# Kernel tuning notes

Hardware: AMD Instinct MI355X
Metric: run time of the kernel (lower is better)

The kernel has to match this reference:

```python
import jax, jax.numpy as jnp
import numpy as np

N_NODES = 100000

def prelu(x, alpha):
    return jnp.where(x >= 0, x, alpha * x)

def setup_inputs() -> dict:
    key = jax.random.key(0)
    ks = jax.random.split(key, 8)
    N, E, D = N_NODES, 1600000, 128
    AX = jax.random.normal(ks[0], (N, D), dtype=jnp.float32)
    A_row = jax.random.randint(ks[1], (E,), 0, N, dtype=jnp.int32)
    A_col = jax.random.randint(ks[2], (E,), 0, N, dtype=jnp.int32)
    A_val = jax.random.uniform(ks[3], (E,), dtype=jnp.float32)
    # Xavier-uniform linear weights, zero bias (as in module init)
    lim = float(np.sqrt(6.0 / (D + D)))
    Wr_w = jax.random.uniform(ks[4], (D, D), minval=-lim, maxval=lim, dtype=jnp.float32)
    W_w = jax.random.uniform(ks[5], (D, D), minval=-lim, maxval=lim, dtype=jnp.float32)
    Wr_b = jnp.zeros((D,), dtype=jnp.float32)
    W_b = jnp.zeros((D,), dtype=jnp.float32)
    g_alpha = jnp.full((1,), 0.25, dtype=jnp.float32)    # PReLU default init
    act_alpha = jnp.full((1,), 0.25, dtype=jnp.float32)
    return {"AX": AX, "A_row": A_row, "A_col": A_col, "A_val": A_val,
            "Wr_w": Wr_w, "Wr_b": Wr_b, "W_w": W_w, "W_b": W_b,
            "g_alpha": g_alpha, "act_alpha": act_alpha}

def reference(AX, A_row, A_col, A_val, Wr_w, Wr_b, W_w, W_b, g_alpha, act_alpha):
    # h = g(Wr @ AX)  : [N, H]
    h = prelu(AX @ Wr_w.T + Wr_b, g_alpha)
    # SpMM: temp[i] = sum_{(i,j) in E} A_val * h[j]
    msgs = A_val[:, None] * h[A_col]                       # [E, H] gather
    temp = jax.ops.segment_sum(msgs, A_row, num_segments=N_NODES)
    # act(W @ temp), unsqueeze batch dim
    out = prelu(temp @ W_w.T + W_b, act_alpha)
    return out[None, :, :]
```

## Files before the change

kernel.cpp:

```cpp
#include <hip/hip_runtime.h>
#include <stdint.h>


typedef _Float16 half8 __attribute__((ext_vector_type(8)));
typedef _Float16 half4 __attribute__((ext_vector_type(4)));
typedef _Float16 half2v __attribute__((ext_vector_type(2)));
typedef float floatx4 __attribute__((ext_vector_type(4)));

#define LDK 136
#define SHIFT 5
#define NBMAX 3200
#define NBLK 256
#define SCT 1024
#define CAP 1024

__global__ __launch_bounds__(SCT)
void bucket_hist(const int* __restrict__ rows, int* __restrict__ hist_g,
                 int E, int chunk, int NB,
                 const float* __restrict__ W, _Float16* __restrict__ W16)
{
    __shared__ int lh[NBMAX];
    int tid = threadIdx.x, blk = blockIdx.x;
    if (blk == 0) {
#pragma unroll
        for (int j = 0; j < 16; ++j) W16[tid + j * 1024] = (_Float16)W[tid + j * 1024];
    }
    for (int i = tid; i < NB; i += SCT) lh[i] = 0;
    __syncthreads();
    int s = blk * chunk, e = min(E, s + chunk);
    for (int i = s + tid; i < e; i += SCT)
        atomicAdd(&lh[rows[i] >> SHIFT], 1);
    __syncthreads();
    for (int b = tid; b < NB; b += SCT)
        hist_g[b * NBLK + blk] = lh[b];
}

__global__ __launch_bounds__(256)
void scan1_fast(int* __restrict__ hist_g, int* __restrict__ tot, int NB)
{
    const int wave = threadIdx.x >> 6;
    const int lane = threadIdx.x & 63;
    const int b = blockIdx.x * 4 + wave;
    if (b >= NB) return;

    int* p = hist_g + b * NBLK + lane * 4;
    int v0 = p[0], v1 = p[1], v2 = p[2], v3 = p[3];
    int s = v0 + v1 + v2 + v3;

    int x = s;
#pragma unroll
    for (int off = 1; off < 64; off <<= 1) {
        int y = __shfl_up(x, off);
        if (lane >= off) x += y;
    }
    int run = x - s;
    p[0] = run; run += v0;
    p[1] = run; run += v1;
    p[2] = run; run += v2;
    p[3] = run;
    if (lane == 63) tot[b] = x;
}

__global__ __launch_bounds__(1024, 4)
void scatter_gemm(const int* __restrict__ rows, const int* __restrict__ cols,
                  const float* __restrict__ vals, const int* __restrict__ tot,
                  const int* __restrict__ hist_g, uint2* __restrict__ edges,
                  int* __restrict__ bkt_ptr, int E, int chunk, int NB,
                  const float* __restrict__ X, const float* __restrict__ Wr,
                  const float* __restrict__ bias, const float* __restrict__ alpha_p,
                  _Float16* __restrict__ out, int N)
{
    __shared__ _Float16 Ws[128 * LDK];
    const int tid = threadIdx.x;

    if (blockIdx.x < NBLK) {
        int* sd  = (int*)Ws;
        int* cur = (int*)Ws + SCT;
        const int blk = blockIdx.x;

        int v[4]; int s = 0;
#pragma unroll
        for (int j = 0; j < 4; ++j) {
            int idx = tid * 4 + j;
            v[j] = (idx < NB) ? tot[idx] : 0;
            s += v[j];
        }
        sd[tid] = s;
        __syncthreads();
        for (int off = 1; off < SCT; off <<= 1) {
            int x = (tid >= off) ? sd[tid - off] : 0;
            __syncthreads();
            sd[tid] += x;
            __syncthreads();
        }
        int base = (tid == 0) ? 0 : sd[tid - 1];
#pragma unroll
        for (int j = 0; j < 4; ++j) {
            int idx = tid * 4 + j;
            if (idx < NB) {
                cur[idx] = base + hist_g[idx * NBLK + blk];
                if (blk == 0) bkt_ptr[idx] = base;
                base += v[j];
            }
        }
        if (blk == 0 && tid == 0) bkt_ptr[NB] = E;
        __syncthreads();

        int s0 = blk * chunk, e0 = min(E, s0 + chunk);
        for (int i = s0 + tid; i < e0; i += SCT) {
            int r = rows[i];
            int b = r >> SHIFT;
            uint2 ed;
            ed.x = (unsigned)cols[i] | ((unsigned)(r & 31) << 20);
            ed.y = __float_as_uint(vals[i]);
            int p = atomicAdd(&cur[b], 1);
            edges[p] = ed;
        }
        return;
    }

    const int bm  = (blockIdx.x - NBLK) * 128;
    const float alpha = *alpha_p;
    const int wave = tid >> 6;
    const int lane = tid & 63;
    const int l15  = lane & 15;
    const int quad = lane >> 4;
    const int mt   = wave >> 1;
    const int nh   = wave & 1;

    half8 a[4];
    {
        const int xrow = bm + mt * 16 + l15;
        const bool ok = xrow < N;
        const float* xp = X + (size_t)xrow * 128 + quad * 8;
#pragma unroll
        for (int k = 0; k < 4; ++k) {
            half8 hv = {};
            if (ok) {
                float4 f0 = *(const float4*)(xp + k * 32);
                float4 f1 = *(const float4*)(xp + k * 32 + 4);
                hv[0] = (_Float16)f0.x; hv[1] = (_Float16)f0.y;
                hv[2] = (_Float16)f0.z; hv[3] = (_Float16)f0.w;
                hv[4] = (_Float16)f1.x; hv[5] = (_Float16)f1.y;
                hv[6] = (_Float16)f1.z; hv[7] = (_Float16)f1.w;
            }
            a[k] = hv;
        }
    }

#pragma unroll
    for (int i = 0; i < 4; ++i) {
        int c   = tid + i * 1024;
        int row = c >> 5;
        int coff = (c & 31) * 4;
        float4 f = *(const float4*)(Wr + row * 128 + coff);
        half4 hv = { (_Float16)f.x, (_Float16)f.y, (_Float16)f.z, (_Float16)f.w };
        *(half4*)(&Ws[row * LDK + coff]) = hv;
    }
    __syncthreads();

    floatx4 acc[4] = {};
#pragma unroll
    for (int k = 0; k < 4; ++k) {
#pragma unroll
        for (int n = 0; n < 4; ++n) {
            int nc = nh * 4 + n;
            half8 b = *(const half8*)(&Ws[(nc * 16 + l15) * LDK + k * 32 + quad * 8]);
            acc[n] = __builtin_amdgcn_mfma_f32_16x16x32_f16(a[k], b, acc[n], 0, 0, 0);
        }
    }

#pragma unroll
    for (int n = 0; n < 4; ++n) {
        int col = (nh * 4 + n) * 16 + l15;
        float bcol = bias[col];
#pragma unroll
        for (int r = 0; r < 4; ++r) {
            int row = bm + mt * 16 + quad * 4 + r;
            if (row < N) {
                float v = acc[n][r] + bcol;
                v = (v >= 0.f) ? v : alpha * v;
                out[(size_t)row * 128 + col] = (_Float16)v;
            }
        }
    }
}

__global__ __launch_bounds__(256, 8)
void spmm_fused(const int* __restrict__ bkt_ptr, const uint2* __restrict__ edges,
                const _Float16* __restrict__ h, const _Float16* __restrict__ W16,
                const float* __restrict__ bias, const float* __restrict__ alpha_p,
                float* __restrict__ out, int N)
{
    __shared__ uint2 eS[CAP];
    __shared__ _Float16 T[32 * LDK];
    __shared__ int bins[32], startS[33];

    const int tid  = threadIdx.x;
    const int wave = tid >> 6;
    const int lane = tid & 63;
    const int b    = blockIdx.x;
    const int s0   = bkt_ptr[b], e0 = bkt_ptr[b + 1];

    float acc[8][2] = {};

    for (int base = s0; base < e0; base += CAP) {
        const int n = min(CAP, e0 - base);
        if (tid < 32) bins[tid] = 0;
        __syncthreads();
        uint2 q[4];
#pragma unroll
        for (int u = 0; u < 4; ++u) {
            int i = tid + u * 256;
            if (i < n) {
                q[u] = edges[base + i];
                atomicAdd(&bins[q[u].x >> 20], 1);
            }
        }
        __syncthreads();
        if (tid < 32) {
            int x = bins[tid];
#pragma unroll
            for (int off = 1; off < 32; off <<= 1) {
                int y = __shfl_up(x, off);
                if (tid >= off) x += y;
            }
            startS[tid + 1] = x;
            if (tid == 0) startS[0] = 0;
            bins[tid] = x - bins[tid];
        }
        __syncthreads();
#pragma unroll
        for (int u = 0; u < 4; ++u) {
            int i = tid + u * 256;
            if (i < n) {
                int p = atomicAdd(&bins[q[u].x >> 20], 1);
                eS[p] = q[u];
            }
        }
        __syncthreads();

#pragma unroll
        for (int j = 0; j < 8; ++j) {
            int r  = wave * 8 + j;
            int rs = startS[r], re = startS[r + 1];
            float a0r = acc[j][0], a1r = acc[j][1];
            int i = rs;
            for (; i + 7 < re; i += 8) {
                uint2 q0 = eS[i],     q1 = eS[i + 1], q2 = eS[i + 2], q3 = eS[i + 3];
                uint2 q4 = eS[i + 4], q5 = eS[i + 5], q6 = eS[i + 6], q7 = eS[i + 7];
                half2v v0 = *(const half2v*)(h + (size_t)(q0.x & 0xFFFFF) * 128 + lane * 2);
                half2v v1 = *(const half2v*)(h + (size_t)(q1.x & 0xFFFFF) * 128 + lane * 2);
                half2v v2 = *(const half2v*)(h + (size_t)(q2.x & 0xFFFFF) * 128 + lane * 2);
                half2v v3 = *(const half2v*)(h + (size_t)(q3.x & 0xFFFFF) * 128 + lane * 2);
                half2v v4 = *(const half2v*)(h + (size_t)(q4.x & 0xFFFFF) * 128 + lane * 2);
                half2v v5 = *(const half2v*)(h + (size_t)(q5.x & 0xFFFFF) * 128 + lane * 2);
                half2v v6 = *(const half2v*)(h + (size_t)(q6.x & 0xFFFFF) * 128 + lane * 2);
                half2v v7 = *(const half2v*)(h + (size_t)(q7.x & 0xFFFFF) * 128 + lane * 2);
                float w0 = __uint_as_float(q0.y), w1 = __uint_as_float(q1.y);
                float w2 = __uint_as_float(q2.y), w3 = __uint_as_float(q3.y);
                float w4 = __uint_as_float(q4.y), w5 = __uint_as_float(q5.y);
                float w6 = __uint_as_float(q6.y), w7 = __uint_as_float(q7.y);
                a0r += w0 * (float)v0[0]; a1r += w0 * (float)v0[1];
                a0r += w1 * (float)v1[0]; a1r += w1 * (float)v1[1];
                a0r += w2 * (float)v2[0]; a1r += w2 * (float)v2[1];
                a0r += w3 * (float)v3[0]; a1r += w3 * (float)v3[1];
                a0r += w4 * (float)v4[0]; a1r += w4 * (float)v4[1];
                a0r += w5 * (float)v5[0]; a1r += w5 * (float)v5[1];
                a0r += w6 * (float)v6[0]; a1r += w6 * (float)v6[1];
                a0r += w7 * (float)v7[0]; a1r += w7 * (float)v7[1];
            }
            for (; i + 1 < re; i += 2) {
                uint2 q0 = eS[i], q1 = eS[i + 1];
                half2v v0 = *(const half2v*)(h + (size_t)(q0.x & 0xFFFFF) * 128 + lane * 2);
                half2v v1 = *(const half2v*)(h + (size_t)(q1.x & 0xFFFFF) * 128 + lane * 2);
                float w0 = __uint_as_float(q0.y), w1 = __uint_as_float(q1.y);
                a0r += w0 * (float)v0[0]; a1r += w0 * (float)v0[1];
                a0r += w1 * (float)v1[0]; a1r += w1 * (float)v1[1];
            }
            if (i < re) {
                uint2 q0 = eS[i];
                half2v v0 = *(const half2v*)(h + (size_t)(q0.x & 0xFFFFF) * 128 + lane * 2);
                float w0 = __uint_as_float(q0.y);
                a0r += w0 * (float)v0[0]; a1r += w0 * (float)v0[1];
            }
            acc[j][0] = a0r; acc[j][1] = a1r;
        }
        __syncthreads();
    }

#pragma unroll
    for (int j = 0; j < 8; ++j) {
        half2v o = { (_Float16)acc[j][0], (_Float16)acc[j][1] };
        *(half2v*)(&T[(wave * 8 + j) * LDK + lane * 2]) = o;
    }
    __syncthreads();

    const float alpha = *alpha_p;
    const int l15  = lane & 15;
    const int quad = lane >> 4;
    floatx4 c[2][2] = {};
#pragma unroll
    for (int k0 = 0; k0 < 128; k0 += 32) {
        half8 a0 = *(const half8*)(&T[(     l15) * LDK + k0 + quad * 8]);
        half8 a1 = *(const half8*)(&T[(16 + l15) * LDK + k0 + quad * 8]);
#pragma unroll
        for (int nt = 0; nt < 2; ++nt) {
            int nrow = (wave * 2 + nt) * 16 + l15;
            half8 bf = *(const half8*)(W16 + nrow * 128 + k0 + quad * 8);
            c[0][nt] = __builtin_amdgcn_mfma_f32_16x16x32_f16(a0, bf, c[0][nt], 0, 0, 0);
            c[1][nt] = __builtin_amdgcn_mfma_f32_16x16x32_f16(a1, bf, c[1][nt], 0, 0, 0);
        }
    }
    const int row0 = b << SHIFT;
#pragma unroll
    for (int mt = 0; mt < 2; ++mt) {
#pragma unroll
        for (int nt = 0; nt < 2; ++nt) {
            int col = (wave * 2 + nt) * 16 + l15;
            float bcol = bias[col];
#pragma unroll
            for (int r = 0; r < 4; ++r) {
                int row = row0 + mt * 16 + quad * 4 + r;
                if (row < N) {
                    float v = c[mt][nt][r] + bcol;
                    v = (v >= 0.f) ? v : alpha * v;
                    out[(size_t)row * 128 + col] = v;
                }
            }
        }
    }
}

static inline size_t align256(size_t x) { return (x + 255) & ~(size_t)255; }

extern "C" void kernel_launch(void* const* d_in, const int* in_sizes, int n_in,
                              void* d_out, int out_size, void* d_ws, size_t ws_size,
                              hipStream_t stream)
{
    const float* AX        = (const float*)d_in[0];
    const int*   A_row     = (const int*)  d_in[1];
    const int*   A_col     = (const int*)  d_in[2];
    const float* A_val     = (const float*)d_in[3];
    const float* Wr_w      = (const float*)d_in[4];
    const float* Wr_b      = (const float*)d_in[5];
    const float* W_w       = (const float*)d_in[6];
    const float* W_b       = (const float*)d_in[7];
    const float* g_alpha   = (const float*)d_in[8];
    const float* act_alpha = (const float*)d_in[9];

    const int N = in_sizes[0] / 128;
    const int E = in_sizes[1];
    const int NB = (N + 31) >> SHIFT;
    const int chunk = (E + NBLK - 1) / NBLK;

    char* ws = (char*)d_ws;
    size_t off = 0;
    _Float16* h       = (_Float16*)(ws + off); off += align256((size_t)N * 128 * 2);
    uint2*    edges   = (uint2*)   (ws + off); off += align256((size_t)E * 8);
    int*      hist_g  = (int*)     (ws + off); off += align256((size_t)NB * NBLK * 4);
    int*      tot     = (int*)     (ws + off); off += align256((size_t)NB * 4);
    int*      bkt_ptr = (int*)     (ws + off); off += align256((size_t)(NB + 1) * 4);
    _Float16* W16     = (_Float16*)(ws + off); off += align256((size_t)128 * 128 * 2);
    (void)ws_size; (void)n_in; (void)out_size;

    const int gemmB = (N + 127) / 128;

    bucket_hist<<<NBLK, SCT, 0, stream>>>(A_row, hist_g, E, chunk, NB, W_w, W16);
    scan1_fast<<<(NB + 3) / 4, 256, 0, stream>>>(hist_g, tot, NB);
    scatter_gemm<<<NBLK + gemmB, 1024, 0, stream>>>(A_row, A_col, A_val, tot, hist_g,
                                                    edges, bkt_ptr, E, chunk, NB,
                                                    AX, Wr_w, Wr_b, g_alpha, h, N);
    spmm_fused<<<NB, 256, 0, stream>>>(bkt_ptr, edges, h, W16, W_b, act_alpha,
                                       (float*)d_out, N);
}
```

Measured before the change: 250.2 us.

## Transpose histogram layout to block-major and tile the column scan; nontemporal edge stores

The per-block bucket histogram is stored block-major, so the histogram writes and the scatter kernel's reads of hist_g are coalesced. The old one-wave-per-bucket scan is replaced by a tiled shared-memory column scan over 64 buckets per block. Edge records are now written as nontemporal 64-bit stores to keep them from polluting cache. The histogram kernels are small next to the SpMM, so any effect is likely minor, and the tiled scan uses more shared memory per block.

```diff
diff --git a/kernel.cpp b/kernel.cpp
--- a/kernel.cpp
+++ b/kernel.cpp
@@ -13,6 +13,8 @@
 #define NBLK 256
 #define SCT 1024
 #define CAP 1024
+#define SCANB 64
+#define NBP 3136
 
 __global__ __launch_bounds__(SCT)
 void bucket_hist(const int* __restrict__ rows, int* __restrict__ hist_g,
@@ -32,33 +34,59 @@
         atomicAdd(&lh[rows[i] >> SHIFT], 1);
     __syncthreads();
     for (int b = tid; b < NB; b += SCT)
-        hist_g[b * NBLK + blk] = lh[b];
+        hist_g[blk * NBP + b] = lh[b];
 }
 
-__global__ __launch_bounds__(256)
-void scan1_fast(int* __restrict__ hist_g, int* __restrict__ tot, int NB)
+__global__ __launch_bounds__(1024)
+void scan1_tile(int* __restrict__ hist_g, int* __restrict__ tot, int NB)
 {
-    const int wave = threadIdx.x >> 6;
-    const int lane = threadIdx.x & 63;
-    const int b = blockIdx.x * 4 + wave;
-    if (b >= NB) return;
-
-    int* p = hist_g + b * NBLK + lane * 4;
-    int v0 = p[0], v1 = p[1], v2 = p[2], v3 = p[3];
-    int s = v0 + v1 + v2 + v3;
-
-    int x = s;
-#pragma unroll
-    for (int off = 1; off < 64; off <<= 1) {
-        int y = __shfl_up(x, off);
-        if (lane >= off) x += y;
-    }
-    int run = x - s;
-    p[0] = run; run += v0;
-    p[1] = run; run += v1;
-    p[2] = run; run += v2;
-    p[3] = run;
-    if (lane == 63) tot[b] = x;
+    __shared__ int tile[NBLK][SCANB + 1];
+    __shared__ int segsum[SCANB][16];
+    const int tid = threadIdx.x;
+    const int b0  = blockIdx.x * SCANB;
+
+#pragma unroll
+    for (int j = 0; j < 16; ++j) {
+        int lin = tid + j * 1024;
+        int r = lin >> 6, c = lin & 63;
+        int gb = b0 + c;
+        tile[r][c] = (gb < NB) ? hist_g[r * NBP + gb] : 0;
+    }
+    __syncthreads();
+
+    const int c = tid >> 4, seg = tid & 15;
+    int s = 0;
+#pragma unroll
+    for (int k = 0; k < 16; ++k) {
+        int r = seg * 16 + k;
+        int v = tile[r][c];
+        tile[r][c] = s;
+        s += v;
+    }
+    segsum[c][seg] = s;
+    __syncthreads();
+    if (seg == 0) {
+        int run = 0;
+#pragma unroll
+        for (int k = 0; k < 16; ++k) { int v = segsum[c][k]; segsum[c][k] = run; run += v; }
+        int gb = b0 + c;
+        if (gb < NB) tot[gb] = run;
+    }
+    __syncthreads();
+    {
+        int base = segsum[c][seg];
+#pragma unroll
+        for (int k = 0; k < 16; ++k) tile[seg * 16 + k][c] += base;
+    }
+    __syncthreads();
+
+#pragma unroll
+    for (int j = 0; j < 16; ++j) {
+        int lin = tid + j * 1024;
+        int r = lin >> 6, cc = lin & 63;
+        int gb = b0 + cc;
+        if (gb < NB) hist_g[r * NBP + gb] = tile[r][cc];
+    }
 }
 
 __global__ __launch_bounds__(1024, 4)
@@ -98,7 +126,7 @@
         for (int j = 0; j < 4; ++j) {
             int idx = tid * 4 + j;
             if (idx < NB) {
-                cur[idx] = base + hist_g[idx * NBLK + blk];
+                cur[idx] = base + hist_g[blk * NBP + idx];
                 if (blk == 0) bkt_ptr[idx] = base;
                 base += v[j];
             }
@@ -110,11 +138,11 @@
         for (int i = s0 + tid; i < e0; i += SCT) {
             int r = rows[i];
             int b = r >> SHIFT;
-            uint2 ed;
-            ed.x = (unsigned)cols[i] | ((unsigned)(r & 31) << 20);
-            ed.y = __float_as_uint(vals[i]);
+            unsigned lo = (unsigned)cols[i] | ((unsigned)(r & 31) << 20);
+            unsigned hi = __float_as_uint(vals[i]);
+            unsigned long long ev = ((unsigned long long)hi << 32) | lo;
             int p = atomicAdd(&cur[b], 1);
-            edges[p] = ed;
+            __builtin_nontemporal_store(ev, (unsigned long long*)(edges + p));
         }
         return;
     }
@@ -358,7 +386,7 @@
     size_t off = 0;
     _Float16* h       = (_Float16*)(ws + off); off += align256((size_t)N * 128 * 2);
     uint2*    edges   = (uint2*)   (ws + off); off += align256((size_t)E * 8);
-    int*      hist_g  = (int*)     (ws + off); off += align256((size_t)NB * NBLK * 4);
+    int*      hist_g  = (int*)     (ws + off); off += align256((size_t)NBLK * NBP * 4);
     int*      tot     = (int*)     (ws + off); off += align256((size_t)NB * 4);
     int*      bkt_ptr = (int*)     (ws + off); off += align256((size_t)(NB + 1) * 4);
     _Float16* W16     = (_Float16*)(ws + off); off += align256((size_t)128 * 128 * 2);
@@ -367,7 +395,7 @@
     const int gemmB = (N + 127) / 128;
 
     bucket_hist<<<NBLK, SCT, 0, stream>>>(A_row, hist_g, E, chunk, NB, W_w, W16);
-    scan1_fast<<<(NB + 3) / 4, 256, 0, stream>>>(hist_g, tot, NB);
+    scan1_tile<<<(NB + SCANB - 1) / SCANB, 1024, 0, stream>>>(hist_g, tot, NB);
     scatter_gemm<<<NBLK + gemmB, 1024, 0, stream>>>(A_row, A_col, A_val, tot, hist_g,
                                                     edges, bkt_ptr, E, chunk, NB,
                                                     AX, Wr_w, Wr_b, g_alpha, h, N);
```

Result: slower. 277.0 us (+10.7%).
